# Performance work log

Measured on AMD Instinct MI355X. Metric: run time of the kernel, lower is better.

The kernel has to match this reference:

```python
import jax, jax.numpy as jnp
import numpy as np

HEAD_SIZE = 64


def setup_inputs() -> dict:
    key = jax.random.key(0)
    ks = jax.random.split(key, 4)
    B, S, H, D = 8, 4096, 768, HEAD_SIZE
    scale = 1.0 / np.sqrt(H)
    return {
        "x": jax.random.normal(ks[0], (B, S, H), dtype=jnp.float32),
        "Wq": jax.random.normal(ks[1], (H, D), dtype=jnp.float32) * scale,
        "bq": jnp.zeros((D,), dtype=jnp.float32),
        "Wk": jax.random.normal(ks[2], (H, D), dtype=jnp.float32) * scale,
        "bk": jnp.zeros((D,), dtype=jnp.float32),
        "Wv": jax.random.normal(ks[3], (H, D), dtype=jnp.float32) * scale,
        "bv": jnp.zeros((D,), dtype=jnp.float32),
    }


def reference(x, Wq, bq, Wk, bk, Wv, bv):
    # x: [B, S, H]
    B, S, H = x.shape
    D = Wq.shape[1]
    q = x @ Wq + bq  # [B, S, D]
    k = x @ Wk + bk
    v = x @ Wv + bv
    # naive full score matrix [B, S, S]
    scores = jnp.einsum("bsd,btd->bst", q, k)
    causal = jnp.tril(jnp.ones((S, S), dtype=bool))  # lower-triangular mask
    scores = jnp.where(causal[None, :, :], scores, -jnp.inf)
    attn = jax.nn.softmax(scores / jnp.sqrt(jnp.float32(D)), axis=-1)
    # dropout is identity in eval/deterministic reference
    out = jnp.einsum("bst,btd->bsd", attn, v)  # [B, S, D]
    return out
```

## Files before the change

kernel.cpp:

```cpp
#include <hip/hip_runtime.h>

typedef unsigned short u16;
typedef __bf16 bf16_t;
typedef bf16_t bf16x8 __attribute__((ext_vector_type(8)));
typedef float f32x4 __attribute__((ext_vector_type(4)));
typedef u16 u16x8 __attribute__((ext_vector_type(8)));
typedef u16 u16x4 __attribute__((ext_vector_type(4)));

#define B_ 8
#define S_ 4096
#define H_ 768
#define M_ (B_ * S_)

__device__ __forceinline__ u16 f2b(float f) {
  unsigned u = __float_as_uint(f);
  u += 0x7fffu + ((u >> 16) & 1u);
  return (u16)(u >> 16);
}

__device__ __forceinline__ void gl_lds16(const void* g, void* l) {
  __builtin_amdgcn_global_load_lds(
      (const __attribute__((address_space(1))) void*)g,
      (__attribute__((address_space(3))) void*)l, 16, 0, 0);
}

__global__ __launch_bounds__(256) void wconv_k(const float* __restrict__ Wq,
                                               const float* __restrict__ Wk,
                                               const float* __restrict__ Wv,
                                               u16* __restrict__ WbT) {
  __shared__ float wt[64 * 68];
  const int tid = threadIdx.x;
  int mat = blockIdx.x / 12;
  int k0 = (blockIdx.x % 12) * 64;
  const float* W = (mat == 0) ? Wq : ((mat == 1) ? Wk : Wv);
  int r = tid >> 2, c0 = (tid & 3) * 16;
  const float* src = W + (size_t)(k0 + r) * 64 + c0;
#pragma unroll
  for (int j = 0; j < 16; j += 4)
    *(float4*)&wt[r * 68 + c0 + j] = *(const float4*)(src + j);
  __syncthreads();
  int d = tid >> 2;
  u16* dst = WbT + (size_t)(mat * 64 + d) * 768 + k0 + c0;
  u16x8 o0, o1;
#pragma unroll
  for (int j = 0; j < 8; ++j) o0[j] = f2b(wt[(c0 + j) * 68 + d]);
#pragma unroll
  for (int j = 0; j < 8; ++j) o1[j] = f2b(wt[(c0 + 8 + j) * 68 + d]);
  *(u16x8*)dst = o0;
  *(u16x8*)(dst + 8) = o1;
}

__global__ __launch_bounds__(256, 4) void qkv_k(const float* __restrict__ x,
                                                const u16* __restrict__ WbT,
                                                const float* __restrict__ bq,
                                                const float* __restrict__ bk,
                                                const float* __restrict__ bv,
                                                u16* __restrict__ qb,
                                                u16* __restrict__ kb,
                                                u16* __restrict__ vbT) {
  __shared__ __align__(16) u16 smem[2 * 1280 + 2 * 7680];
  const int tid = threadIdx.x;
  const int w = tid >> 6, ln = tid & 15, qd = (tid >> 4) & 3;
  const int row0 = blockIdx.x * 32;

  const f32x4 z4 = {0.f, 0.f, 0.f, 0.f};
  f32x4 acc[2][3];
#pragma unroll
  for (int rt = 0; rt < 2; ++rt)
#pragma unroll
    for (int ct = 0; ct < 3; ++ct) acc[rt][ct] = z4;

  const int xr = tid >> 3, xc = (tid & 7) * 4;
  float4 xf;
  u16x8 wf[3];

  auto load_t = [&](int kt) {
    xf = *(const float4*)(x + (size_t)(row0 + xr) * 768 + kt * 32 + xc);
#pragma unroll
    for (int i = 0; i < 3; ++i) {
      int c = i * 256 + tid;
      int r = c >> 2, off = (c & 3) * 8;
      wf[i] = *(const u16x8*)(WbT + (size_t)r * 768 + kt * 32 + off);
    }
  };
  auto write_b = [&](int kt) {
    u16* xs = smem + (kt & 1) * 1280;
    u16* wsb = smem + 2560 + (kt & 1) * 7680;
    u16x4 v;
    v[0] = f2b(xf.x); v[1] = f2b(xf.y); v[2] = f2b(xf.z); v[3] = f2b(xf.w);
    *(u16x4*)&xs[xr * 40 + xc] = v;
#pragma unroll
    for (int i = 0; i < 3; ++i) {
      int c = i * 256 + tid;
      int r = c >> 2, off = (c & 3) * 8;
      *(u16x8*)&wsb[r * 40 + off] = wf[i];
    }
  };

  load_t(0);
  write_b(0);
  load_t(1);
  for (int kt = 0; kt < 24; ++kt) {
    __syncthreads();
    if (kt < 23) {
      write_b(kt + 1);
      if (kt < 22) load_t(kt + 2);
    }
    u16* xs = smem + (kt & 1) * 1280;
    u16* wsb = smem + 2560 + (kt & 1) * 7680;
    bf16x8 af[2], bfr[3];
#pragma unroll
    for (int rt = 0; rt < 2; ++rt)
      af[rt] = *(const bf16x8*)&xs[(rt * 16 + ln) * 40 + qd * 8];
#pragma unroll
    for (int ct = 0; ct < 3; ++ct)
      bfr[ct] = *(const bf16x8*)&wsb[(w * 48 + ct * 16 + ln) * 40 + qd * 8];
#pragma unroll
    for (int rt = 0; rt < 2; ++rt)
#pragma unroll
      for (int ct = 0; ct < 3; ++ct)
        acc[rt][ct] = __builtin_amdgcn_mfma_f32_16x16x32_bf16(
            af[rt], bfr[ct], acc[rt][ct], 0, 0, 0);
  }
  __syncthreads();

  u16* vt = smem;
#pragma unroll
  for (int ct = 0; ct < 3; ++ct) {
    int col = w * 48 + ct * 16 + ln;
    int mat = col >> 6, d = col & 63;
    if (mat < 2) {
      const float* bp = (mat == 0) ? bq : bk;
      u16* op = (mat == 0) ? qb : kb;
      float bias = bp[d];
      float scale = (mat == 0) ? 0.18033688011112042f : 1.0f;
#pragma unroll
      for (int rt = 0; rt < 2; ++rt)
#pragma unroll
        for (int r = 0; r < 4; ++r)
          op[(size_t)(row0 + rt * 16 + qd * 4 + r) * 64 + d] =
              f2b((acc[rt][ct][r] + bias) * scale);
    } else {
      float bias = bv[d];
#pragma unroll
      for (int rt = 0; rt < 2; ++rt)
#pragma unroll
        for (int r = 0; r < 4; ++r)
          vt[d * 40 + rt * 16 + qd * 4 + r] = f2b(acc[rt][ct][r] + bias);
    }
  }
  __syncthreads();
  {
    int d = tid >> 2, so = (tid & 3) * 8;
    int b = row0 >> 12, s0 = row0 & 4095;
    *(u16x8*)(vbT + ((size_t)b * 64 + d) * 4096 + s0 + so) =
        *(const u16x8*)&vt[d * 40 + so];
  }
}

__global__ __launch_bounds__(256, 3) void attn_k(const u16* __restrict__ qb,
                                                 const u16* __restrict__ kb,
                                                 const u16* __restrict__ vbT,
                                                 u16* __restrict__ po,
                                                 float* __restrict__ pl) {
  __shared__ __align__(16) u16 ks[2][4096];
  __shared__ __align__(16) u16 vs[2][4096];
  __shared__ __align__(16) u16 ps[4 * 16 * 72];
  const int tid = threadIdx.x;
  const int w = tid >> 6, ln = tid & 15, qd = (tid >> 4) & 3;
  const int id = blockIdx.x;
  const int b = id & 7;
  int t = id >> 3;
  int qi = 31, rem = t;
  for (;;) {
    int c = (2 * qi + 9) >> 3;
    if (rem < c) break;
    rem -= c;
    --qi;
  }
  const int chunk = rem;
  const int tstart = rem * 8;
  int tcount = 2 * qi + 2 - tstart;
  if (tcount > 8) tcount = 8;
  const int q0 = qi * 128, q0w = q0 + w * 32;
  const int base = b * S_;
  const u16* kg = kb + (size_t)base * 64;
  const u16* vg = vbT + (size_t)b * 64 * 4096;

  bf16x8 qf[2][2];
#pragma unroll
  for (int qt = 0; qt < 2; ++qt) {
    const u16* qrow = qb + (size_t)(base + q0w + qt * 16 + ln) * 64;
    qf[qt][0] = *(const bf16x8*)(qrow + qd * 8);
    qf[qt][1] = *(const bf16x8*)(qrow + 32 + qd * 8);
  }
  const f32x4 z4 = {0.f, 0.f, 0.f, 0.f};
  f32x4 o[2][4];
#pragma unroll
  for (int qt = 0; qt < 2; ++qt)
#pragma unroll
    for (int nt = 0; nt < 4; ++nt) o[qt][nt] = z4;
  float lp[2] = {0.f, 0.f};
  u16* psw = ps + w * (16 * 72);
  const int lr = (tid & 63) >> 3, csl = tid & 7;

  auto prefetch = [&](int bufi, int tile) {
    const u16* kt_ = kg + (size_t)tile * 4096;
    const u16* vt_ = vg + tile * 64;
#pragma unroll
    for (int i = 0; i < 2; ++i) {
      int r0 = w * 16 + i * 8;
      int r = r0 + lr;
      int c = csl ^ (r & 7);
      gl_lds16(kt_ + r * 64 + c * 8, &ks[bufi][r0 * 64]);
      gl_lds16(vt_ + (size_t)r * 4096 + c * 8, &vs[bufi][r0 * 64]);
    }
  };

  prefetch(0, tstart);
  int buf = 0;
  for (int it = 0; it < tcount; ++it) {
    __syncthreads();
    if (it + 1 < tcount) prefetch(buf ^ 1, tstart + it + 1);
    const int t0a = (tstart + it) * 64;

    bf16x8 kf[2][4], vf[2][4];
#pragma unroll
    for (int kc = 0; kc < 2; ++kc) {
      int cs = ((kc * 4 + qd) ^ (ln & 7)) * 8;
#pragma unroll
      for (int nt = 0; nt < 4; ++nt) {
        kf[kc][nt] = *(const bf16x8*)&ks[buf][(nt * 16 + ln) * 64 + cs];
        vf[kc][nt] = *(const bf16x8*)&vs[buf][(nt * 16 + ln) * 64 + cs];
      }
    }
#pragma unroll
    for (int qt = 0; qt < 2; ++qt) {
      f32x4 s[4] = {z4, z4, z4, z4};
#pragma unroll
      for (int kc = 0; kc < 2; ++kc)
#pragma unroll
        for (int nt = 0; nt < 4; ++nt)
          s[nt] = __builtin_amdgcn_mfma_f32_16x16x32_bf16(kf[kc][nt], qf[qt][kc],
                                                          s[nt], 0, 0, 0);
      if (t0a + 63 > q0w + qt * 16) {
#pragma unroll
        for (int nt = 0; nt < 4; ++nt) {
          int tg = t0a + nt * 16 + qd * 4;
          int qg = q0w + qt * 16 + ln;
#pragma unroll
          for (int r = 0; r < 4; ++r)
            if (tg + r > qg) s[nt][r] = -INFINITY;
        }
      }
#pragma unroll
      for (int nt = 0; nt < 4; ++nt) {
        u16x4 pk;
#pragma unroll
        for (int r = 0; r < 4; ++r) {
          float p = __builtin_amdgcn_exp2f(s[nt][r]);
          lp[qt] += p;
          pk[r] = f2b(p);
        }
        *(u16x4*)&psw[ln * 72 + nt * 16 + qd * 4] = pk;
      }
#pragma unroll
      for (int kc = 0; kc < 2; ++kc) {
        bf16x8 pf = *(const bf16x8*)&psw[ln * 72 + kc * 32 + qd * 8];
#pragma unroll
        for (int nt = 0; nt < 4; ++nt)
          o[qt][nt] = __builtin_amdgcn_mfma_f32_16x16x32_bf16(vf[kc][nt], pf,
                                                              o[qt][nt], 0, 0, 0);
      }
    }
    buf ^= 1;
  }

  u16* poc = po + (size_t)chunk * M_ * 64;
  float* plc = pl + (size_t)chunk * M_;
#pragma unroll
  for (int qt = 0; qt < 2; ++qt) {
    float v = lp[qt];
    v += __shfl_xor(v, 16);
    v += __shfl_xor(v, 32);
    int row = base + q0w + qt * 16 + ln;
#pragma unroll
    for (int nt = 0; nt < 4; ++nt) {
      u16x4 ov;
#pragma unroll
      for (int r = 0; r < 4; ++r) ov[r] = f2b(o[qt][nt][r]);
      *(u16x4*)&poc[(size_t)row * 64 + nt * 16 + qd * 4] = ov;
    }
    if (qd == 0) plc[row] = v;
  }
}

__global__ __launch_bounds__(256) void comb_k(const u16* __restrict__ po,
                                              const float* __restrict__ pl,
                                              float* __restrict__ out) {
  int idx = blockIdx.x * 256 + threadIdx.x;
  int r = idx >> 4, d0 = (idx & 15) * 4;
  int qi = (r & 4095) >> 7;
  int nch = (2 * qi + 9) >> 3;
  float4 a = {0.f, 0.f, 0.f, 0.f};
  float l = 0.f;
  for (int c = 0; c < nch; ++c) {
    u16x4 p = *(const u16x4*)(po + ((size_t)c * M_ + r) * 64 + d0);
    a.x += __uint_as_float((unsigned)p[0] << 16);
    a.y += __uint_as_float((unsigned)p[1] << 16);
    a.z += __uint_as_float((unsigned)p[2] << 16);
    a.w += __uint_as_float((unsigned)p[3] << 16);
    l += pl[(size_t)c * M_ + r];
  }
  float inv = 1.0f / l;
  a.x *= inv; a.y *= inv; a.z *= inv; a.w *= inv;
  *(float4*)(out + (size_t)r * 64 + d0) = a;
}

extern "C" void kernel_launch(void* const* d_in, const int* in_sizes, int n_in,
                              void* d_out, int out_size, void* d_ws, size_t ws_size,
                              hipStream_t stream) {
  const float* x  = (const float*)d_in[0];
  const float* Wq = (const float*)d_in[1];
  const float* bq = (const float*)d_in[2];
  const float* Wk = (const float*)d_in[3];
  const float* bk = (const float*)d_in[4];
  const float* Wv = (const float*)d_in[5];
  const float* bv = (const float*)d_in[6];
  float* out = (float*)d_out;

  char* wsp = (char*)d_ws;
  u16* WbT  = (u16*)wsp;
  u16* qb   = (u16*)(wsp + 294912);
  u16* kb   = (u16*)(wsp + 4489216);
  u16* vbT  = (u16*)(wsp + 8683520);
  u16* po   = (u16*)(wsp + 12877824);
  float* pl = (float*)(wsp + 46432256);

  hipLaunchKernelGGL(wconv_k, dim3(36), dim3(256), 0, stream, Wq, Wk, Wv, WbT);
  hipLaunchKernelGGL(qkv_k, dim3(1024), dim3(256), 0, stream,
                     x, WbT, bq, bk, bv, qb, kb, vbT);
  hipLaunchKernelGGL(attn_k, dim3(1152), dim3(256), 0, stream,
                     qb, kb, vbT, po, pl);
  hipLaunchKernelGGL(comb_k, dim3(2048), dim3(256), 0, stream, po, pl, out);
}
```

Before: 242.2 us.

## Tile V-transpose layout and use direct-to-LDS DMA for weights and KV tiles

The QKV projection now stores V transposed in contiguous 64x64 tiles, so each attention K/V tile becomes one contiguous 8KB block instead of 64 strided rows. The weight operand in qkv_k is now loaded with global_load_lds into a swizzled single buffer, replacing the register staging and double buffering. The attention loop now issues DMA for two tiles at once, syncs, computes both, then syncs again, instead of prefetching the next tile while computing the current one. This lowers the register and LDS traffic for staging and improves V load locality, but it removes the overlap of loads with compute in both kernels.

```diff
diff --git a/kernel.cpp b/kernel.cpp
--- a/kernel.cpp
+++ b/kernel.cpp
@@ -57,8 +57,9 @@
                                                 const float* __restrict__ bv,
                                                 u16* __restrict__ qb,
                                                 u16* __restrict__ kb,
-                                                u16* __restrict__ vbT) {
-  __shared__ __align__(16) u16 smem[2 * 1280 + 2 * 7680];
+                                                u16* __restrict__ vbT2) {
+  __shared__ __align__(16) u16 xs[32 * 40];
+  __shared__ __align__(16) u16 wsd[192 * 32];
   const int tid = threadIdx.x;
   const int w = tid >> 6, ln = tid & 15, qd = (tid >> 4) & 3;
   const int row0 = blockIdx.x * 32;
@@ -72,59 +73,52 @@
 
   const int xr = tid >> 3, xc = (tid & 7) * 4;
   float4 xf;
-  u16x8 wf[3];
-
-  auto load_t = [&](int kt) {
+  const int dl = tid & 63;
+  const int dr = dl >> 2;
+  const int dsl = dl & 3;
+  auto load_x = [&](int kt) {
     xf = *(const float4*)(x + (size_t)(row0 + xr) * 768 + kt * 32 + xc);
-#pragma unroll
-    for (int i = 0; i < 3; ++i) {
-      int c = i * 256 + tid;
-      int r = c >> 2, off = (c & 3) * 8;
-      wf[i] = *(const u16x8*)(WbT + (size_t)r * 768 + kt * 32 + off);
-    }
   };
-  auto write_b = [&](int kt) {
-    u16* xs = smem + (kt & 1) * 1280;
-    u16* wsb = smem + 2560 + (kt & 1) * 7680;
-    u16x4 v;
-    v[0] = f2b(xf.x); v[1] = f2b(xf.y); v[2] = f2b(xf.z); v[3] = f2b(xf.w);
-    *(u16x4*)&xs[xr * 40 + xc] = v;
-#pragma unroll
-    for (int i = 0; i < 3; ++i) {
-      int c = i * 256 + tid;
-      int r = c >> 2, off = (c & 3) * 8;
-      *(u16x8*)&wsb[r * 40 + off] = wf[i];
+  auto dma_w = [&](int kt) {
+#pragma unroll
+    for (int j = 0; j < 3; ++j) {
+      int row = j * 64 + w * 16 + dr;
+      int ch = dsl ^ (row & 3);
+      gl_lds16(WbT + (size_t)row * 768 + kt * 32 + ch * 8,
+               &wsd[(j * 64 + w * 16) * 32]);
     }
   };
 
-  load_t(0);
-  write_b(0);
-  load_t(1);
+  load_x(0);
   for (int kt = 0; kt < 24; ++kt) {
+    dma_w(kt);
+    {
+      u16x4 v;
+      v[0] = f2b(xf.x); v[1] = f2b(xf.y); v[2] = f2b(xf.z); v[3] = f2b(xf.w);
+      *(u16x4*)&xs[xr * 40 + xc] = v;
+    }
+    if (kt < 23) load_x(kt + 1);
     __syncthreads();
-    if (kt < 23) {
-      write_b(kt + 1);
-      if (kt < 22) load_t(kt + 2);
-    }
-    u16* xs = smem + (kt & 1) * 1280;
-    u16* wsb = smem + 2560 + (kt & 1) * 7680;
     bf16x8 af[2], bfr[3];
 #pragma unroll
     for (int rt = 0; rt < 2; ++rt)
       af[rt] = *(const bf16x8*)&xs[(rt * 16 + ln) * 40 + qd * 8];
 #pragma unroll
-    for (int ct = 0; ct < 3; ++ct)
-      bfr[ct] = *(const bf16x8*)&wsb[(w * 48 + ct * 16 + ln) * 40 + qd * 8];
+    for (int ct = 0; ct < 3; ++ct) {
+      int row = w * 48 + ct * 16 + ln;
+      int slot = qd ^ (row & 3);
+      bfr[ct] = *(const bf16x8*)&wsd[row * 32 + slot * 8];
+    }
 #pragma unroll
     for (int rt = 0; rt < 2; ++rt)
 #pragma unroll
       for (int ct = 0; ct < 3; ++ct)
         acc[rt][ct] = __builtin_amdgcn_mfma_f32_16x16x32_bf16(
             af[rt], bfr[ct], acc[rt][ct], 0, 0, 0);
-  }
-  __syncthreads();
-
-  u16* vt = smem;
+    __syncthreads();
+  }
+
+  u16* vt = wsd;
 #pragma unroll
   for (int ct = 0; ct < 3; ++ct) {
     int col = w * 48 + ct * 16 + ln;
@@ -152,19 +146,19 @@
   __syncthreads();
   {
     int d = tid >> 2, so = (tid & 3) * 8;
-    int b = row0 >> 12, s0 = row0 & 4095;
-    *(u16x8*)(vbT + ((size_t)b * 64 + d) * 4096 + s0 + so) =
-        *(const u16x8*)&vt[d * 40 + so];
+    int b = row0 >> 12, ti = (row0 & 4095) >> 6, th = row0 & 63;
+    u16* dst = vbT2 + (size_t)(b * 64 + ti) * 4096 + d * 64 + th + so;
+    *(u16x8*)dst = *(const u16x8*)&vt[d * 40 + so];
   }
 }
 
 __global__ __launch_bounds__(256, 3) void attn_k(const u16* __restrict__ qb,
                                                  const u16* __restrict__ kb,
-                                                 const u16* __restrict__ vbT,
+                                                 const u16* __restrict__ vbT2,
                                                  u16* __restrict__ po,
                                                  float* __restrict__ pl) {
-  __shared__ __align__(16) u16 ks[2][4096];
-  __shared__ __align__(16) u16 vs[2][4096];
+  __shared__ __align__(16) u16 ks[2 * 4096];
+  __shared__ __align__(16) u16 vs[2 * 4096];
   __shared__ __align__(16) u16 ps[4 * 16 * 72];
   const int tid = threadIdx.x;
   const int w = tid >> 6, ln = tid & 15, qd = (tid >> 4) & 3;
@@ -185,7 +179,7 @@
   const int q0 = qi * 128, q0w = q0 + w * 32;
   const int base = b * S_;
   const u16* kg = kb + (size_t)base * 64;
-  const u16* vg = vbT + (size_t)b * 64 * 4096;
+  const u16* vg = vbT2 + (size_t)b * 64 * 4096;
 
   bf16x8 qf[2][2];
 #pragma unroll
@@ -204,34 +198,28 @@
   u16* psw = ps + w * (16 * 72);
   const int lr = (tid & 63) >> 3, csl = tid & 7;
 
-  auto prefetch = [&](int bufi, int tile) {
+  auto dma_tile = [&](int slot, int tile) {
     const u16* kt_ = kg + (size_t)tile * 4096;
-    const u16* vt_ = vg + tile * 64;
+    const u16* vt_ = vg + (size_t)tile * 4096;
 #pragma unroll
     for (int i = 0; i < 2; ++i) {
       int r0 = w * 16 + i * 8;
       int r = r0 + lr;
       int c = csl ^ (r & 7);
-      gl_lds16(kt_ + r * 64 + c * 8, &ks[bufi][r0 * 64]);
-      gl_lds16(vt_ + (size_t)r * 4096 + c * 8, &vs[bufi][r0 * 64]);
+      gl_lds16(kt_ + r * 64 + c * 8, &ks[slot * 4096 + r0 * 64]);
+      gl_lds16(vt_ + r * 64 + c * 8, &vs[slot * 4096 + r0 * 64]);
     }
   };
 
-  prefetch(0, tstart);
-  int buf = 0;
-  for (int it = 0; it < tcount; ++it) {
-    __syncthreads();
-    if (it + 1 < tcount) prefetch(buf ^ 1, tstart + it + 1);
-    const int t0a = (tstart + it) * 64;
-
+  auto sub = [&](int slot, int t0a) {
     bf16x8 kf[2][4], vf[2][4];
 #pragma unroll
     for (int kc = 0; kc < 2; ++kc) {
       int cs = ((kc * 4 + qd) ^ (ln & 7)) * 8;
 #pragma unroll
       for (int nt = 0; nt < 4; ++nt) {
-        kf[kc][nt] = *(const bf16x8*)&ks[buf][(nt * 16 + ln) * 64 + cs];
-        vf[kc][nt] = *(const bf16x8*)&vs[buf][(nt * 16 + ln) * 64 + cs];
+        kf[kc][nt] = *(const bf16x8*)&ks[slot * 4096 + (nt * 16 + ln) * 64 + cs];
+        vf[kc][nt] = *(const bf16x8*)&vs[slot * 4096 + (nt * 16 + ln) * 64 + cs];
       }
     }
 #pragma unroll
@@ -273,7 +261,16 @@
                                                               o[qt][nt], 0, 0, 0);
       }
     }
-    buf ^= 1;
+  };
+
+  for (int it = 0; it < tcount; it += 2) {
+    const int t0 = tstart + it;
+    dma_tile(0, t0);
+    if (it + 1 < tcount) dma_tile(1, t0 + 1);
+    __syncthreads();
+    sub(0, t0 * 64);
+    if (it + 1 < tcount) sub(1, (t0 + 1) * 64);
+    __syncthreads();
   }
 
   u16* poc = po + (size_t)chunk * M_ * 64;
@@ -333,14 +330,14 @@
   u16* WbT  = (u16*)wsp;
   u16* qb   = (u16*)(wsp + 294912);
   u16* kb   = (u16*)(wsp + 4489216);
-  u16* vbT  = (u16*)(wsp + 8683520);
+  u16* vbT2 = (u16*)(wsp + 8683520);
   u16* po   = (u16*)(wsp + 12877824);
   float* pl = (float*)(wsp + 46432256);
 
   hipLaunchKernelGGL(wconv_k, dim3(36), dim3(256), 0, stream, Wq, Wk, Wv, WbT);
   hipLaunchKernelGGL(qkv_k, dim3(1024), dim3(256), 0, stream,
-                     x, WbT, bq, bk, bv, qb, kb, vbT);
+                     x, WbT, bq, bk, bv, qb, kb, vbT2);
   hipLaunchKernelGGL(attn_k, dim3(1152), dim3(256), 0, stream,
-                     qb, kb, vbT, po, pl);
+                     qb, kb, vbT2, po, pl);
   hipLaunchKernelGGL(comb_k, dim3(2048), dim3(256), 0, stream, po, pl, out);
 }
```

New measurement: 265.6 us. +9.7%, slower.
